# Kernel optimization log

Measured on AMD Instinct MI355X. Metric: run time of the kernel, lower is better.

## Reference

```python
import jax, jax.numpy as jnp
import numpy as np

BN_EPS = 1e-5
C = 128  # channels (hardcoded by feed_forward convs)


def _bn(v, gamma, beta, mean, var):
    # BatchNorm1d in inference form over channel axis of [B, C, N]
    scale = gamma / jnp.sqrt(var + BN_EPS)
    return (v - mean[:, None]) * scale[:, None] + beta[:, None]


def setup_inputs() -> dict:
    key = jax.random.key(0)
    ks = jax.random.split(key, 8)
    B, N = 8, 2048
    s = 0.05
    return {
        "x": jax.random.normal(ks[0], (B, N, C), jnp.float32),
        "Wq": jax.random.normal(ks[1], (C // 4, C), jnp.float32) * s,
        "Wk": jax.random.normal(ks[2], (C // 4, C), jnp.float32) * s,
        "Wv": jax.random.normal(ks[3], (C, C), jnp.float32) * s,
        "bv": jnp.zeros((C,), jnp.float32),
        "Wt": jax.random.normal(ks[4], (C, C), jnp.float32) * s,
        "bt": jnp.zeros((C,), jnp.float32),
        "g1": jnp.ones((C,), jnp.float32),
        "b1": jnp.zeros((C,), jnp.float32),
        "m1": jnp.zeros((C,), jnp.float32),
        "v1": jnp.ones((C,), jnp.float32),
        "W1": jax.random.normal(ks[5], (512, C), jnp.float32) * s,
        "bf1": jnp.zeros((512,), jnp.float32),
        "W2": jax.random.normal(ks[6], (C, 512), jnp.float32) * s,
        "bf2": jnp.zeros((C,), jnp.float32),
        "g2": jnp.ones((C,), jnp.float32),
        "b2": jnp.zeros((C,), jnp.float32),
        "m2": jnp.zeros((C,), jnp.float32),
        "v2": jnp.ones((C,), jnp.float32),
    }


def reference(x, Wq, Wk, Wv, bv, Wt, bt, g1, b1, m1, v1,
              W1, bf1, W2, bf2, g2, b2, m2, v2):
    # x: [B, N, C] -> work in [B, C, N] layout like the torch module
    xc = jnp.transpose(x, (0, 2, 1))                      # [B, C, N]
    # q_conv(x).permute -> [B, N, C/4]; k_conv -> [B, C/4, N]
    x_q = jnp.einsum('bnc,oc->bno', x, Wq)                # [B, N, C/4]
    x_k = jnp.einsum('bnc,oc->bon', x, Wk)                # [B, C/4, N]
    x_v = jnp.einsum('bnc,oc->bon', x, Wv) + bv[:, None]  # [B, C, N]

    energy = jnp.einsum('bnd,bdm->bnm', x_q, x_k)         # [B, N, N]
    scale = jnp.sqrt(jnp.asarray(C, x.dtype))             # sqrt(x_v.shape[-2])
    attention = jax.nn.softmax(energy / scale, axis=-1)   # [B, N, N]
    x_r = jnp.einsum('bcn,bnm->bcm', x_v, attention)      # [B, C, N]

    t = jnp.einsum('oc,bcn->bon', Wt, xc - x_r) + bt[:, None]
    x_r2 = jax.nn.relu(_bn(t, g1, b1, m1, v1))
    h = xc + x_r2                                         # [B, C, N]

    residual = h
    f = jax.nn.relu(jnp.einsum('oc,bcn->bon', W1, h) + bf1[:, None])
    f = jnp.einsum('of,bfn->bon', W2, f) + bf2[:, None]
    out = _bn(residual + f, g2, b2, m2, v2)               # [B, C, N]
    return jnp.transpose(out, (0, 2, 1))                  # [B, N, C]
```

## Files before the change

kernel.cpp:

```cpp
#include <hip/hip_runtime.h>
#include <hip/hip_bf16.h>

#define BDIM 256
#define NPTS (8 * 2048)
#define CC 128
#define DD 32
#define FF 512
#define NN 2048
#define SCALE 0.08838834764831845f

typedef float f32x4 __attribute__((ext_vector_type(4)));
typedef short s16x8 __attribute__((ext_vector_type(8)));
typedef unsigned short ushort_t;

__device__ __forceinline__ ushort_t bf16r(float x) {
    __hip_bfloat16 h = __float2bfloat16(x);
    return *reinterpret_cast<ushort_t*>(&h);
}
__device__ __forceinline__ float bf16tof(ushort_t u) {
    unsigned v = ((unsigned)u) << 16;
    return *reinterpret_cast<float*>(&v);
}
__device__ __forceinline__ unsigned pack2(float a, float b) {
    return ((unsigned)bf16r(b) << 16) | (unsigned)bf16r(a);
}

__global__ void k_cvt_all(const float* __restrict__ W1, const float* __restrict__ W2,
                          const float* __restrict__ Wq, const float* __restrict__ Wk,
                          const float* __restrict__ Wv, const float* __restrict__ Wt,
                          ushort_t* __restrict__ dst) {
    int i = blockIdx.x * BDIM + threadIdx.x;
    const float* src; int off;
    if (i < 16384)      { src = W1; off = 0; }
    else if (i < 32768) { src = W2; off = 16384; }
    else if (i < 33792) { src = Wq; off = 32768; }
    else if (i < 34816) { src = Wk; off = 33792; }
    else if (i < 38912) { src = Wv; off = 34816; }
    else                { src = Wt; off = 38912; }
    float4 v = ((const float4*)src)[i - off];
    *(uint2*)(dst + (long)i * 4) = make_uint2(pack2(v.x, v.y), pack2(v.z, v.w));
}

__global__ __launch_bounds__(256) void k_proj(
        const float* __restrict__ x, const ushort_t* __restrict__ Wb,
        const float* __restrict__ bv,
        ushort_t* __restrict__ qg, ushort_t* __restrict__ kg,
        ushort_t* __restrict__ vTg) {
    __shared__ ushort_t xs[32][136];
    __shared__ ushort_t qks[32][72];
    __shared__ ushort_t vs[32][136];
    long base = (long)blockIdx.x * 32;
    int b = (int)(base >> 11);
    int n0 = (int)(base & (NN - 1));
    int t = threadIdx.x, w = t >> 6, l = t & 63, a = l & 15, g = l >> 4;
    {
        const float4* xg4 = (const float4*)(x + base * CC);
        #pragma unroll
        for (int rep = 0; rep < 4; ++rep) {
            int i = rep * BDIM + t;
            float4 v4 = xg4[i];
            int p = i >> 5, c4 = (i & 31) * 4;
            *(uint2*)&xs[p][c4] = make_uint2(pack2(v4.x, v4.y), pack2(v4.z, v4.w));
        }
    }
    s16x8 bF[3][4];
    #pragma unroll
    for (int ct = 0; ct < 3; ++ct) {
        int ctg = w * 3 + ct;
        #pragma unroll
        for (int ki = 0; ki < 4; ++ki)
            bF[ct][ki] = *(const s16x8*)(Wb + ((long)(ctg * 16 + a)) * CC + ki * 32 + g * 8);
    }
    __syncthreads();
    #pragma unroll
    for (int rt = 0; rt < 2; ++rt) {
        s16x8 aF[4];
        #pragma unroll
        for (int ki = 0; ki < 4; ++ki)
            aF[ki] = *(const s16x8*)&xs[rt * 16 + a][ki * 32 + g * 8];
        #pragma unroll
        for (int ct = 0; ct < 3; ++ct) {
            f32x4 acc = (f32x4){0.f, 0.f, 0.f, 0.f};
            #pragma unroll
            for (int ki = 0; ki < 4; ++ki)
                acc = __builtin_amdgcn_mfma_f32_16x16x32_bf16(aF[ki], bF[ct][ki], acc, 0, 0, 0);
            int ctg = w * 3 + ct;
            int oc = ctg * 16 + a;
            float bias = (oc >= 64) ? bv[oc - 64] : 0.f;
            #pragma unroll
            for (int r = 0; r < 4; ++r) {
                int p = rt * 16 + g * 4 + r;
                float val = acc[r] + bias;
                if (oc < 64) qks[p][oc] = bf16r(val);
                else         vs[p][oc - 64] = bf16r(val);
            }
        }
    }
    __syncthreads();
    {
        int p = t >> 3, c = (t & 7) * 4;
        *(uint2*)(qg + (base + p) * DD + c) = *(const uint2*)&qks[p][c];
        *(uint2*)(kg + (base + p) * DD + c) = *(const uint2*)&qks[p][32 + c];
    }
    #pragma unroll
    for (int rep = 0; rep < 2; ++rep) {
        int i = rep * BDIM + t;
        int c = i & 127, nch = i >> 7;
        int p0 = nch * 8;
        uint4 r;
        r.x = (unsigned)vs[p0+0][c] | ((unsigned)vs[p0+1][c] << 16);
        r.y = (unsigned)vs[p0+2][c] | ((unsigned)vs[p0+3][c] << 16);
        r.z = (unsigned)vs[p0+4][c] | ((unsigned)vs[p0+5][c] << 16);
        r.w = (unsigned)vs[p0+6][c] | ((unsigned)vs[p0+7][c] << 16);
        *(uint4*)(vTg + ((long)(b * CC + c)) * NN + n0 + p0) = r;
    }
}

__global__ __launch_bounds__(256) void k_rowstats(
        const ushort_t* __restrict__ qg, const ushort_t* __restrict__ kg,
        float* __restrict__ rowinv) {
    __shared__ float ps[4][64];
    int b = blockIdx.x >> 5;
    int nt = (blockIdx.x & 31) * 64;
    int t = threadIdx.x, w = t >> 6, l = t & 63, a = l & 15, g = l >> 4;
    s16x8 qA[4];
    #pragma unroll
    for (int s = 0; s < 4; ++s)
        qA[s] = *(const s16x8*)(qg + ((long)(b * NN + nt + s*16 + a)) * DD + g*8);
    float sm[16];
    #pragma unroll
    for (int i = 0; i < 16; ++i) sm[i] = 0.f;
    s16x8 kB = *(const s16x8*)(kg + ((long)(b * NN + w * 16 + a)) * DD + g*8);
    for (int it = 0; it < 32; ++it) {
        s16x8 kBn;
        if (it < 31)
            kBn = *(const s16x8*)(kg + ((long)(b * NN + ((it+1)*4 + w)*16 + a)) * DD + g*8);
        #pragma unroll
        for (int s = 0; s < 4; ++s) {
            f32x4 D = (f32x4){0.f, 0.f, 0.f, 0.f};
            D = __builtin_amdgcn_mfma_f32_16x16x32_bf16(qA[s], kB, D, 0, 0, 0);
            #pragma unroll
            for (int r = 0; r < 4; ++r)
                sm[s * 4 + r] += __expf(D[r] * SCALE);
        }
        kB = kBn;
    }
    #pragma unroll
    for (int off = 1; off < 16; off <<= 1)
        #pragma unroll
        for (int ix = 0; ix < 16; ++ix)
            sm[ix] += __shfl_xor(sm[ix], off, 64);
    if (a == 0) {
        #pragma unroll
        for (int s = 0; s < 4; ++s)
            #pragma unroll
            for (int r = 0; r < 4; ++r)
                ps[w][s * 16 + g * 4 + r] = sm[s * 4 + r];
    }
    __syncthreads();
    if (t < 64) {
        float S = ps[0][t] + ps[1][t] + ps[2][t] + ps[3][t];
        rowinv[(long)b * NN + nt + t] = 1.f / S;
    }
}

__global__ __launch_bounds__(512) void k_pv(
        const ushort_t* __restrict__ qg, const ushort_t* __restrict__ kg,
        const ushort_t* __restrict__ vTg, const float* __restrict__ rowinv,
        const float* __restrict__ x, const ushort_t* __restrict__ Wtb,
        const float* __restrict__ bt,
        const float* __restrict__ g1, const float* __restrict__ b1,
        const float* __restrict__ m1, const float* __restrict__ v1,
        ushort_t* __restrict__ hb) {
    __shared__ __align__(16) char arena[77824];
    auto vTs   = (ushort_t (*)[128][72])(arena);
    auto qs    = (ushort_t (*)[64][40])(arena + 55296);
    auto ks    = (ushort_t (*)[40])(arena + 65536);
    auto pT    = (ushort_t (*)[32][72])(arena + 68096);
    auto rin_s = (float (*)[64])(arena + 77312);
    int b = blockIdx.x >> 6;
    int m0 = (blockIdx.x & 63) * 32;
    int t = threadIdx.x, w = t >> 6, l = t & 63, a = l & 15, g = l >> 4;
    int nsub = w & 3, msub = w >> 2;
    const ushort_t* vTb = vTg + (long)b * CC * NN;
    if (t < 128) {
        int r = t >> 2, o = (t & 3) * 8;
        *(s16x8*)&ks[r][o] = *(const s16x8*)(kg + ((long)(b * NN + m0 + r)) * DD + o);
    }
    int qr = t >> 2, qo = (t & 3) * 8;
    int c0 = t >> 3, vo0 = (t & 7) * 8;
    int c1 = (512 + t) >> 3, vo1 = (t & 7) * 8;
    uint4 qreg = make_uint4(0, 0, 0, 0), vreg0, vreg1;
    float rinreg = 0.f;
    if (t < 256) qreg = *(const uint4*)(qg + ((long)(b * NN + qr)) * DD + qo);
    vreg0 = *(const uint4*)(vTb + (long)c0 * NN + vo0);
    vreg1 = *(const uint4*)(vTb + (long)c1 * NN + vo1);
    if (t < 64) rinreg = rowinv[(long)b * NN + t];
    if (t < 256) *(uint4*)&qs[0][qr][qo] = qreg;
    *(uint4*)&vTs[0][c0][vo0] = vreg0;
    *(uint4*)&vTs[0][c1][vo1] = vreg1;
    if (t < 64) rin_s[0][t] = rinreg;
    f32x4 acc[2];
    acc[0] = (f32x4){0.f, 0.f, 0.f, 0.f};
    acc[1] = (f32x4){0.f, 0.f, 0.f, 0.f};
    __syncthreads();
    for (int it = 0; it <= 32; ++it) {
        if (it < 31) {
            int ntn = (it + 1) * 64;
            if (t < 256) qreg = *(const uint4*)(qg + ((long)(b * NN + ntn + qr)) * DD + qo);
            vreg0 = *(const uint4*)(vTb + (long)c0 * NN + ntn + vo0);
            vreg1 = *(const uint4*)(vTb + (long)c1 * NN + ntn + vo1);
            if (t < 64) rinreg = rowinv[(long)b * NN + ntn + t];
        }
        if (it < 32) {
            int bq = it & 1;
            s16x8 qf = *(const s16x8*)&qs[bq][nsub * 16 + a][g * 8];
            s16x8 kf = *(const s16x8*)&ks[msub * 16 + a][g * 8];
            f32x4 e = (f32x4){0.f, 0.f, 0.f, 0.f};
            e = __builtin_amdgcn_mfma_f32_16x16x32_bf16(qf, kf, e, 0, 0, 0);
            float p[4];
            #pragma unroll
            for (int r = 0; r < 4; ++r)
                p[r] = __expf(e[r] * SCALE) * rin_s[bq][nsub * 16 + g * 4 + r];
            *(uint2*)&pT[bq][msub * 16 + a][nsub * 16 + g * 4] =
                make_uint2(pack2(p[0], p[1]), pack2(p[2], p[3]));
        }
        if (it >= 1) {
            int pb = (it - 1) & 1;
            int vb = (it - 1) % 3;
            #pragma unroll
            for (int k2 = 0; k2 < 2; ++k2) {
                s16x8 A0 = *(const s16x8*)&pT[pb][a][k2 * 32 + g * 8];
                s16x8 A1 = *(const s16x8*)&pT[pb][16 + a][k2 * 32 + g * 8];
                s16x8 Bf = *(const s16x8*)&vTs[vb][w * 16 + a][k2 * 32 + g * 8];
                acc[0] = __builtin_amdgcn_mfma_f32_16x16x32_bf16(A0, Bf, acc[0], 0, 0, 0);
                acc[1] = __builtin_amdgcn_mfma_f32_16x16x32_bf16(A1, Bf, acc[1], 0, 0, 0);
            }
        }
        if (it < 31) {
            int bn = (it + 1) & 1;
            int vn = (it + 1) % 3;
            if (t < 256) *(uint4*)&qs[bn][qr][qo] = qreg;
            *(uint4*)&vTs[vn][c0][vo0] = vreg0;
            *(uint4*)&vTs[vn][c1][vo1] = vreg1;
            if (t < 64) rin_s[bn][t] = rinreg;
        }
        __syncthreads();
    }
    auto xb  = (ushort_t (*)[136])(arena);
    auto dsx = (ushort_t (*)[136])(arena + 8704);
    long pbase = (long)b * NN + m0;
    {
        const float4* xg4 = (const float4*)(x + pbase * CC);
        #pragma unroll
        for (int rep = 0; rep < 2; ++rep) {
            int i = rep * 512 + t;
            float4 xv = xg4[i];
            int p = i >> 5, c4 = (i & 31) * 4;
            *(uint2*)&xb[p][c4] = make_uint2(pack2(xv.x, xv.y), pack2(xv.z, xv.w));
        }
    }
    __syncthreads();
    #pragma unroll
    for (int ms = 0; ms < 2; ++ms)
        #pragma unroll
        for (int r = 0; r < 4; ++r) {
            int ml = ms * 16 + g * 4 + r;
            int c = w * 16 + a;
            dsx[ml][c] = bf16r(bf16tof(xb[ml][c]) - acc[ms][r]);
        }
    __syncthreads();
    {
        int ph = w & 1, fh = w >> 1;
        s16x8 aF[4];
        #pragma unroll
        for (int ki = 0; ki < 4; ++ki)
            aF[ki] = *(const s16x8*)&dsx[ph * 16 + a][ki * 32 + g * 8];
        #pragma unroll
        for (int oi = 0; oi < 2; ++oi) {
            int ot = fh * 2 + oi;
            f32x4 ac = (f32x4){0.f, 0.f, 0.f, 0.f};
            #pragma unroll
            for (int ki = 0; ki < 4; ++ki) {
                s16x8 bF = *(const s16x8*)(Wtb + ((long)(ot * 16 + a)) * CC + ki * 32 + g * 8);
                ac = __builtin_amdgcn_mfma_f32_16x16x32_bf16(aF[ki], bF, ac, 0, 0, 0);
            }
            int o = ot * 16 + a;
            float sc = g1[o] * rsqrtf(v1[o] + 1e-5f);
            float mm = m1[o], bb = b1[o], bo = bt[o];
            #pragma unroll
            for (int r = 0; r < 4; ++r) {
                int p = ph * 16 + g * 4 + r;
                float tv = ((ac[r] + bo) - mm) * sc + bb;
                tv = fmaxf(tv, 0.f);
                hb[(pbase + p) * CC + o] = bf16r(bf16tof(xb[p][o]) + tv);
            }
        }
    }
}

__global__ __launch_bounds__(256) void k_ff(
        const ushort_t* __restrict__ hb, const ushort_t* __restrict__ W1b,
        const ushort_t* __restrict__ W2b,
        const float* __restrict__ bf1, const float* __restrict__ bf2,
        const float* __restrict__ g2, const float* __restrict__ b2,
        const float* __restrict__ m2, const float* __restrict__ v2,
        float* __restrict__ out) {
    __shared__ ushort_t hs[32][136];
    __shared__ ushort_t w1s[2][64][128];
    __shared__ ushort_t w2s[2][128][64];
    __shared__ ushort_t fss[32][72];
    long pbase = (long)blockIdx.x * 32;
    int t = threadIdx.x;
    int l = t & 63, wid = t >> 6;
    int ph = wid & 1, fh = wid >> 1;
    int lr = l & 15, lg = l >> 4;
    for (int i = t; i < 512; i += BDIM) {
        int r = i >> 4, c0 = (i & 15) * 8;
        *(uint4*)&hs[r][c0] = *(const uint4*)(hb + (pbase + r) * CC + c0);
    }
    #pragma unroll
    for (int rep = 0; rep < 4; ++rep) {
        int i = rep * BDIM + t;
        int r = i >> 4, c0 = (i & 15) * 8;
        *(uint4*)&w1s[0][r][c0 ^ ((r & 7) * 8)] = *(const uint4*)(W1b + (long)r * CC + c0);
    }
    #pragma unroll
    for (int rep = 0; rep < 4; ++rep) {
        int i = rep * BDIM + t;
        int r = i >> 3, c0 = (i & 7) * 8;
        *(uint4*)&w2s[0][r][c0 ^ ((r & 7) * 8)] = *(const uint4*)(W2b + (long)r * FF + c0);
    }
    __syncthreads();
    s16x8 hA[4];
    #pragma unroll
    for (int ki = 0; ki < 4; ++ki)
        hA[ki] = *(const s16x8*)&hs[ph * 16 + lr][ki * 32 + lg * 8];
    f32x4 acc2[4];
    #pragma unroll
    for (int i = 0; i < 4; ++i) acc2[i] = (f32x4){0.f, 0.f, 0.f, 0.f};

    int cur = 0;
    uint4 wrg0, wrg1, wrg2, wrg3, wrg4, wrg5, wrg6, wrg7;
    for (int fc = 0; fc < 8; ++fc) {
        if (fc) __syncthreads();
        int f0 = fc * 64;
        if (fc < 7) {
            int f0n = f0 + 64;
            int r1 = t >> 4, c1 = (t & 15) * 8;
            int r2 = t >> 3, c2 = (t & 7) * 8;
            wrg0 = *(const uint4*)(W1b + (long)(f0n + r1) * CC + c1);
            wrg1 = *(const uint4*)(W1b + (long)(f0n + 16 + r1) * CC + c1);
            wrg2 = *(const uint4*)(W1b + (long)(f0n + 32 + r1) * CC + c1);
            wrg3 = *(const uint4*)(W1b + (long)(f0n + 48 + r1) * CC + c1);
            wrg4 = *(const uint4*)(W2b + (long)r2 * FF + f0n + c2);
            wrg5 = *(const uint4*)(W2b + (long)(32 + r2) * FF + f0n + c2);
            wrg6 = *(const uint4*)(W2b + (long)(64 + r2) * FF + f0n + c2);
            wrg7 = *(const uint4*)(W2b + (long)(96 + r2) * FF + f0n + c2);
        }
        #pragma unroll
        for (int fi = 0; fi < 2; ++fi) {
            int ft = fh * 2 + fi;
            int row = ft * 16 + lr;
            f32x4 a1 = (f32x4){0.f, 0.f, 0.f, 0.f};
            #pragma unroll
            for (int ki = 0; ki < 4; ++ki) {
                int col = ki * 32 + lg * 8;
                s16x8 bfr = *(const s16x8*)&w1s[cur][row][col ^ ((row & 7) * 8)];
                a1 = __builtin_amdgcn_mfma_f32_16x16x32_bf16(hA[ki], bfr, a1, 0, 0, 0);
            }
            float bias = bf1[f0 + ft * 16 + lr];
            #pragma unroll
            for (int r = 0; r < 4; ++r) {
                float vv = fmaxf(a1[r] + bias, 0.f);
                fss[ph * 16 + lg * 4 + r][ft * 16 + lr] = bf16r(vv);
            }
        }
        __syncthreads();
        #pragma unroll
        for (int k2 = 0; k2 < 2; ++k2) {
            s16x8 afr = *(const s16x8*)&fss[ph * 16 + lr][k2 * 32 + lg * 8];
            #pragma unroll
            for (int oi = 0; oi < 4; ++oi) {
                int ot = fh * 4 + oi;
                int row = ot * 16 + lr;
                int col = k2 * 32 + lg * 8;
                s16x8 bfr = *(const s16x8*)&w2s[cur][row][col ^ ((row & 7) * 8)];
                acc2[oi] = __builtin_amdgcn_mfma_f32_16x16x32_bf16(afr, bfr, acc2[oi], 0, 0, 0);
            }
        }
        if (fc < 7) {
            int nb = cur ^ 1;
            int r1 = t >> 4, c1 = (t & 15) * 8;
            int r2 = t >> 3, c2 = (t & 7) * 8;
            *(uint4*)&w1s[nb][r1][c1 ^ ((r1 & 7) * 8)] = wrg0;
            *(uint4*)&w1s[nb][16 + r1][c1 ^ ((r1 & 7) * 8)] = wrg1;
            *(uint4*)&w1s[nb][32 + r1][c1 ^ ((r1 & 7) * 8)] = wrg2;
            *(uint4*)&w1s[nb][48 + r1][c1 ^ ((r1 & 7) * 8)] = wrg3;
            *(uint4*)&w2s[nb][r2][c2 ^ ((r2 & 7) * 8)] = wrg4;
            *(uint4*)&w2s[nb][32 + r2][c2 ^ (((32 + r2) & 7) * 8)] = wrg5;
            *(uint4*)&w2s[nb][64 + r2][c2 ^ (((64 + r2) & 7) * 8)] = wrg6;
            *(uint4*)&w2s[nb][96 + r2][c2 ^ (((96 + r2) & 7) * 8)] = wrg7;
            cur = nb;
        }
    }
    #pragma unroll
    for (int oi = 0; oi < 4; ++oi) {
        int o = (fh * 4 + oi) * 16 + lr;
        float sc = g2[o] * rsqrtf(v2[o] + 1e-5f);
        float mm = m2[o], bb = b2[o], bias2 = bf2[o];
        #pragma unroll
        for (int r = 0; r < 4; ++r) {
            int p = ph * 16 + lg * 4 + r;
            float val = bf16tof(hs[p][o]) + acc2[oi][r] + bias2;
            out[(pbase + p) * CC + o] = (val - mm) * sc + bb;
        }
    }
}

extern "C" void kernel_launch(void* const* d_in, const int* in_sizes, int n_in,
                              void* d_out, int out_size, void* d_ws, size_t ws_size,
                              hipStream_t stream) {
    const float* x   = (const float*)d_in[0];
    const float* Wq  = (const float*)d_in[1];
    const float* Wk  = (const float*)d_in[2];
    const float* Wv  = (const float*)d_in[3];
    const float* bv  = (const float*)d_in[4];
    const float* Wt  = (const float*)d_in[5];
    const float* bt  = (const float*)d_in[6];
    const float* g1  = (const float*)d_in[7];
    const float* b1  = (const float*)d_in[8];
    const float* m1  = (const float*)d_in[9];
    const float* v1  = (const float*)d_in[10];
    const float* W1  = (const float*)d_in[11];
    const float* bf1 = (const float*)d_in[12];
    const float* W2  = (const float*)d_in[13];
    const float* bf2 = (const float*)d_in[14];
    const float* g2  = (const float*)d_in[15];
    const float* b2  = (const float*)d_in[16];
    const float* m2  = (const float*)d_in[17];
    const float* v2  = (const float*)d_in[18];
    float* out = (float*)d_out;

    float* ws  = (float*)d_ws;
    float* rin = ws;
    ushort_t* qg   = (ushort_t*)(rin + NPTS);
    ushort_t* kg   = qg + (long)NPTS * DD;
    ushort_t* vTg  = kg + (long)NPTS * DD;
    ushort_t* hbuf = vTg + (long)NPTS * CC;
    ushort_t* W1b  = hbuf + (long)NPTS * CC;
    ushort_t* W2b  = W1b + FF * CC;
    ushort_t* Wb   = W2b + FF * CC;
    ushort_t* Wtb  = Wb + 192 * CC;

    k_cvt_all<<<168, BDIM, 0, stream>>>(W1, W2, Wq, Wk, Wv, Wt, W1b);
    k_proj<<<NPTS / 32, BDIM, 0, stream>>>(x, Wb, bv, qg, kg, vTg);
    k_rowstats<<<8 * (NN / 64), BDIM, 0, stream>>>(qg, kg, rin);
    k_pv<<<8 * (NN / 32), 512, 0, stream>>>(qg, kg, vTg, rin,
                                            x, Wtb, bt, g1, b1, m1, v1, hbuf);
    k_ff<<<NPTS / 32, BDIM, 0, stream>>>(hbuf, W1b, W2b, bf1, bf2, g2, b2, m2, v2, out);
}
```

Measured before the change: 78.83 us.

## Load Q, K, V and row-inverse fragments directly from global into registers in k_pv

```diff
diff --git a/kernel.cpp b/kernel.cpp
--- a/kernel.cpp
+++ b/kernel.cpp
@@ -172,79 +172,59 @@
         const float* __restrict__ g1, const float* __restrict__ b1,
         const float* __restrict__ m1, const float* __restrict__ v1,
         ushort_t* __restrict__ hb) {
-    __shared__ __align__(16) char arena[77824];
-    auto vTs   = (ushort_t (*)[128][72])(arena);
-    auto qs    = (ushort_t (*)[64][40])(arena + 55296);
-    auto ks    = (ushort_t (*)[40])(arena + 65536);
-    auto pT    = (ushort_t (*)[32][72])(arena + 68096);
-    auto rin_s = (float (*)[64])(arena + 77312);
+    __shared__ __align__(16) char arena[17408];
+    auto pT = (ushort_t (*)[32][72])(arena);
     int b = blockIdx.x >> 6;
     int m0 = (blockIdx.x & 63) * 32;
     int t = threadIdx.x, w = t >> 6, l = t & 63, a = l & 15, g = l >> 4;
     int nsub = w & 3, msub = w >> 2;
     const ushort_t* vTb = vTg + (long)b * CC * NN;
-    if (t < 128) {
-        int r = t >> 2, o = (t & 3) * 8;
-        *(s16x8*)&ks[r][o] = *(const s16x8*)(kg + ((long)(b * NN + m0 + r)) * DD + o);
-    }
-    int qr = t >> 2, qo = (t & 3) * 8;
-    int c0 = t >> 3, vo0 = (t & 7) * 8;
-    int c1 = (512 + t) >> 3, vo1 = (t & 7) * 8;
-    uint4 qreg = make_uint4(0, 0, 0, 0), vreg0, vreg1;
-    float rinreg = 0.f;
-    if (t < 256) qreg = *(const uint4*)(qg + ((long)(b * NN + qr)) * DD + qo);
-    vreg0 = *(const uint4*)(vTb + (long)c0 * NN + vo0);
-    vreg1 = *(const uint4*)(vTb + (long)c1 * NN + vo1);
-    if (t < 64) rinreg = rowinv[(long)b * NN + t];
-    if (t < 256) *(uint4*)&qs[0][qr][qo] = qreg;
-    *(uint4*)&vTs[0][c0][vo0] = vreg0;
-    *(uint4*)&vTs[0][c1][vo1] = vreg1;
-    if (t < 64) rin_s[0][t] = rinreg;
+    s16x8 kf = *(const s16x8*)(kg + ((long)(b * NN + m0 + msub * 16 + a)) * DD + g * 8);
+    const ushort_t* qrow = qg + ((long)(b * NN + nsub * 16 + a)) * DD + g * 8;
+    const float*    rrow = rowinv + (long)b * NN + nsub * 16 + g * 4;
+    int c = w * 16 + a;
+    const ushort_t* vrow = vTb + (long)c * NN + g * 8;
+    s16x8 qf_c = *(const s16x8*)qrow;
+    float4 rr_c = *(const float4*)rrow;
+    s16x8 qf_n; float4 rr_n;
+    s16x8 bf_use0, bf_use1, bf_ld0, bf_ld1;
     f32x4 acc[2];
     acc[0] = (f32x4){0.f, 0.f, 0.f, 0.f};
     acc[1] = (f32x4){0.f, 0.f, 0.f, 0.f};
-    __syncthreads();
     for (int it = 0; it <= 32; ++it) {
+        if (it < 32) {
+            f32x4 e = (f32x4){0.f, 0.f, 0.f, 0.f};
+            e = __builtin_amdgcn_mfma_f32_16x16x32_bf16(qf_c, kf, e, 0, 0, 0);
+            float p0 = __expf(e[0] * SCALE) * rr_c.x;
+            float p1 = __expf(e[1] * SCALE) * rr_c.y;
+            float p2 = __expf(e[2] * SCALE) * rr_c.z;
+            float p3 = __expf(e[3] * SCALE) * rr_c.w;
+            *(uint2*)&pT[it & 1][msub * 16 + a][nsub * 16 + g * 4] =
+                make_uint2(pack2(p0, p1), pack2(p2, p3));
+        }
         if (it < 31) {
-            int ntn = (it + 1) * 64;
-            if (t < 256) qreg = *(const uint4*)(qg + ((long)(b * NN + ntn + qr)) * DD + qo);
-            vreg0 = *(const uint4*)(vTb + (long)c0 * NN + ntn + vo0);
-            vreg1 = *(const uint4*)(vTb + (long)c1 * NN + ntn + vo1);
-            if (t < 64) rinreg = rowinv[(long)b * NN + ntn + t];
+            long off = (long)(it + 1) * 64;
+            qf_n = *(const s16x8*)(qrow + off * DD);
+            rr_n = *(const float4*)(rrow + off);
         }
         if (it < 32) {
-            int bq = it & 1;
-            s16x8 qf = *(const s16x8*)&qs[bq][nsub * 16 + a][g * 8];
-            s16x8 kf = *(const s16x8*)&ks[msub * 16 + a][g * 8];
-            f32x4 e = (f32x4){0.f, 0.f, 0.f, 0.f};
-            e = __builtin_amdgcn_mfma_f32_16x16x32_bf16(qf, kf, e, 0, 0, 0);
-            float p[4];
-            #pragma unroll
-            for (int r = 0; r < 4; ++r)
-                p[r] = __expf(e[r] * SCALE) * rin_s[bq][nsub * 16 + g * 4 + r];
-            *(uint2*)&pT[bq][msub * 16 + a][nsub * 16 + g * 4] =
-                make_uint2(pack2(p[0], p[1]), pack2(p[2], p[3]));
+            long off = (long)it * 64;
+            bf_ld0 = *(const s16x8*)(vrow + off);
+            bf_ld1 = *(const s16x8*)(vrow + off + 32);
         }
         if (it >= 1) {
             int pb = (it - 1) & 1;
-            int vb = (it - 1) % 3;
-            #pragma unroll
-            for (int k2 = 0; k2 < 2; ++k2) {
-                s16x8 A0 = *(const s16x8*)&pT[pb][a][k2 * 32 + g * 8];
-                s16x8 A1 = *(const s16x8*)&pT[pb][16 + a][k2 * 32 + g * 8];
-                s16x8 Bf = *(const s16x8*)&vTs[vb][w * 16 + a][k2 * 32 + g * 8];
-                acc[0] = __builtin_amdgcn_mfma_f32_16x16x32_bf16(A0, Bf, acc[0], 0, 0, 0);
-                acc[1] = __builtin_amdgcn_mfma_f32_16x16x32_bf16(A1, Bf, acc[1], 0, 0, 0);
-            }
-        }
-        if (it < 31) {
-            int bn = (it + 1) & 1;
-            int vn = (it + 1) % 3;
-            if (t < 256) *(uint4*)&qs[bn][qr][qo] = qreg;
-            *(uint4*)&vTs[vn][c0][vo0] = vreg0;
-            *(uint4*)&vTs[vn][c1][vo1] = vreg1;
-            if (t < 64) rin_s[bn][t] = rinreg;
-        }
+            s16x8 A00 = *(const s16x8*)&pT[pb][a][g * 8];
+            s16x8 A10 = *(const s16x8*)&pT[pb][16 + a][g * 8];
+            s16x8 A01 = *(const s16x8*)&pT[pb][a][32 + g * 8];
+            s16x8 A11 = *(const s16x8*)&pT[pb][16 + a][32 + g * 8];
+            acc[0] = __builtin_amdgcn_mfma_f32_16x16x32_bf16(A00, bf_use0, acc[0], 0, 0, 0);
+            acc[1] = __builtin_amdgcn_mfma_f32_16x16x32_bf16(A10, bf_use0, acc[1], 0, 0, 0);
+            acc[0] = __builtin_amdgcn_mfma_f32_16x16x32_bf16(A01, bf_use1, acc[0], 0, 0, 0);
+            acc[1] = __builtin_amdgcn_mfma_f32_16x16x32_bf16(A11, bf_use1, acc[1], 0, 0, 0);
+        }
+        bf_use0 = bf_ld0; bf_use1 = bf_ld1;
+        qf_c = qf_n; rr_c = rr_n;
         __syncthreads();
     }
     auto xb  = (ushort_t (*)[136])(arena);
@@ -266,7 +246,6 @@
         #pragma unroll
         for (int r = 0; r < 4; ++r) {
             int ml = ms * 16 + g * 4 + r;
-            int c = w * 16 + a;
             dsx[ml][c] = bf16r(bf16tof(xb[ml][c]) - acc[ms][r]);
         }
     __syncthreads();
```

Measured after the change: 88.87 us. +12.7%, slower.
